# Performance work log

Measured on AMD Instinct MI355X. Metric: run time of the kernel, lower is better.

The kernel has to match this reference:

```python
import jax, jax.numpy as jnp
import numpy as np


def setup_inputs() -> dict:
    key = jax.random.key(0)
    ks = jax.random.split(key, 5)
    B, D, W = 8, 768, 128
    scale = 1.0 / np.sqrt(D)
    return {
        "x": jax.random.normal(ks[0], (B, D, W, W), dtype=jnp.float32),
        "in_proj_w": jax.random.normal(ks[1], (3 * D, D), dtype=jnp.float32) * scale,
        "in_proj_b": jax.random.normal(ks[2], (3 * D,), dtype=jnp.float32) * 0.01,
        "out_w": jax.random.normal(ks[3], (D, D), dtype=jnp.float32) * scale,
        "out_b": jax.random.normal(ks[4], (D,), dtype=jnp.float32) * 0.01,
        "num_heads": 12,
        "num_tokens": 8,
    }


def reference(x, in_proj_w, in_proj_b, out_w, out_b, num_heads, num_tokens):
    B, D, Wd, Hd = x.shape
    nt = num_tokens
    gs = Hd // nt            # grid (block) size
    T = nt * nt              # number of blocks / queries
    S = gs * gs              # k/v tokens per block
    h = num_heads
    hd = D // h

    # ---- query: adaptive avg pool to (nt, nt), flatten, permute -> (B, T, D)
    q = x.reshape(B, D, nt, gs, nt, gs).mean(axis=(3, 5))      # (B, D, nt, nt)
    q = q.reshape(B, D, T).transpose(0, 2, 1)                   # (B, T, D)

    # ---- key/value: faithful reproduction of unfold + view(x.size()) + reshape
    # torch: kv_perm (B,W,H,D) -> unfold -> (B, nt, nt, D, gs, gs) contiguous,
    # then reinterpreted flat as (B, W*H, D) (scrambles channel/pixel layout).
    t = x.transpose(0, 2, 3, 1)                                 # (B, W, H, D)
    t = t.reshape(B, nt, gs, nt, gs, D).transpose(0, 1, 3, 5, 2, 4)  # (B,nt,nt,D,gs,gs)
    kv = t.reshape(B, T, S, D)                                  # chunked into T blocks of S tokens

    # ---- in-projections (torch MultiheadAttention packed weights)
    Wq, Wk, Wv = in_proj_w[:D], in_proj_w[D:2 * D], in_proj_w[2 * D:]
    bq, bk, bv = in_proj_b[:D], in_proj_b[D:2 * D], in_proj_b[2 * D:]
    qp = (q @ Wq.T + bq).reshape(B, T, h, hd)                   # (B, T, h, hd)
    kp = (kv @ Wk.T + bk).reshape(B, T, S, h, hd)               # (B, T, S, h, hd)
    vp = (kv @ Wv.T + bv).reshape(B, T, S, h, hd)

    # ---- block-local single-query attention, batched over all T blocks
    scores = jnp.einsum("bthd,btshd->bths", qp, kp) / np.sqrt(hd)  # (B, T, h, S)
    attn = jax.nn.softmax(scores, axis=-1)
    ctx = jnp.einsum("bths,btshd->bthd", attn, vp).reshape(B, T, D)

    # ---- out projection
    return ctx @ out_w.T + out_b                                # (B, T, D)
```

## Files before the change

### kernel.cpp

```cpp
#include <hip/hip_runtime.h>
#include <hip/hip_bf16.h>

#define D_ 768
#define W_ 128
#define T_ 64
#define S_ 256
#define H_ 12
#define BT_ 512

typedef __attribute__((ext_vector_type(8))) short short8v;
typedef __attribute__((ext_vector_type(4))) float f32x4;

__device__ __forceinline__ unsigned short f2bf(float f) {
  unsigned u = __float_as_uint(f);
  u = (u + 0x7FFFu + ((u >> 16) & 1u)) >> 16;
  return (unsigned short)u;
}
__device__ __forceinline__ float bfu(unsigned s) {
  return __uint_as_float(s << 16);
}

__global__ __launch_bounds__(384) void k_pack(const float* __restrict__ x,
                                              unsigned short* __restrict__ packed,
                                              float* __restrict__ q) {
  const int blk  = blockIdx.x;
  const int cc   = blk & 15;
  const int tjp  = (blk >> 4) & 3;
  const int ti   = (blk >> 6) & 7;
  const int b    = blk >> 9;
  const int tid  = threadIdx.x;
  const int c8   = tid & 7;
  const int ch   = tid >> 3;
  const int btl  = c8 >> 2;
  const int btg0 = b*64 + ti*8 + tjp*2;
  const int ch0  = cc * 48;

  __shared__ unsigned short tile[48][2][264];
  __shared__ float poolsc[48][2];

  const float* xcol = x + (size_t)b*D_*16384 + (size_t)(ch0 + ch)*16384
                        + (16*ti)*128 + 32*tjp + c8*4;

  float psum = 0.f;
  #pragma unroll
  for (int r = 0; r < 16; ++r) {
    const float4 v = *(const float4*)(xcol + r*128);
    const int px = r*16 + (c8 & 3)*4;
    unsigned lo = (unsigned)f2bf(v.x) | ((unsigned)f2bf(v.y) << 16);
    unsigned hi = (unsigned)f2bf(v.z) | ((unsigned)f2bf(v.w) << 16);
    *(uint2*)&tile[ch][btl][px] = make_uint2(lo, hi);
    psum += (v.x + v.y) + (v.z + v.w);
  }
  psum += __shfl_xor(psum, 1);
  psum += __shfl_xor(psum, 2);
  if ((c8 & 3) == 0) poolsc[ch][btl] = psum;
  __syncthreads();

  for (int ii = tid; ii < 3072; ii += 384) {
    const int btl2 = ii / 1536;
    const int r2   = ii - btl2*1536;
    const int sl   = r2 / 96;
    const int r3   = r2 - sl*96;
    const int c    = r3 >> 5;
    const int p8   = r3 & 31;
    const int chs  = sl*3 + c;
    const uint4 v = *(const uint4*)&tile[chs][btl2][p8*8];
    unsigned short* dst = packed + (size_t)(btg0 + btl2)*(S_*D_)
                        + (size_t)(cc*16 + sl)*D_ + c*256 + p8*8;
    *(uint4*)dst = v;
  }
  if (tid < 96) {
    const int ch2 = tid >> 1, bl = tid & 1;
    q[(size_t)(btg0 + bl)*D_ + ch0 + ch2] = poolsc[ch2][bl] * (1.0f/256.0f);
  }
}

__global__ __launch_bounds__(256) void k_qp(const float* __restrict__ q,
                                            const float* __restrict__ ipw,
                                            const float* __restrict__ ipb,
                                            float* __restrict__ qp) {
  const int jt = blockIdx.x >> 6;
  const int bt0 = (blockIdx.x & 63) * 8;
  const int tid = threadIdx.x;
  const float* Wr = ipw + (size_t)jt*64*D_;
  __shared__ float wt[64][65];
  __shared__ float at[8][65];
  const int i = tid & 63, qw = tid >> 6;
  float acc[2] = {0,0};
  for (int dc = 0; dc < D_; dc += 64) {
    #pragma unroll
    for (int k = 0; k < 4; ++k) {
      const int idx = k*256 + tid;
      const int r = idx >> 4, c4 = idx & 15;
      *(float4*)&wt[r][c4*4] = *(const float4*)(Wr + (size_t)r*D_ + dc + c4*4);
    }
    if (tid < 128) {
      const int r = tid >> 4, c4 = tid & 15;
      *(float4*)&at[r][c4*4] = *(const float4*)(q + (size_t)(bt0 + r)*D_ + dc + c4*4);
    }
    __syncthreads();
    #pragma unroll
    for (int dd = 0; dd < 64; ++dd) {
      const float wv = wt[i][dd];
      #pragma unroll
      for (int k = 0; k < 2; ++k)
        acc[k] += at[qw + k*4][dd] * wv;
    }
    __syncthreads();
  }
  const float bqv = ipb[jt*64 + i];
  #pragma unroll
  for (int k = 0; k < 2; ++k)
    qp[(size_t)(bt0 + qw + k*4)*D_ + jt*64 + i] = acc[k] + bqv;
}

__global__ __launch_bounds__(256) void k_fold(const float* __restrict__ qp,
                                              const float* __restrict__ ipw,
                                              unsigned short* __restrict__ qkout) {
  const int btc = blockIdx.x & 15;
  const int nt  = blockIdx.x >> 4;
  const int h   = nt / 12;
  const int ddc = (nt % 12) * 64;
  const int bt0 = btc * 32;
  const int tid = threadIdx.x;
  __shared__ float qpl[32][68];
  __shared__ float wkl[64][68];
  #pragma unroll
  for (int k = 0; k < 2; ++k) {
    const int idx = k*256 + tid;
    const int r = idx >> 4, c4 = idx & 15;
    *(float4*)&qpl[r][c4*4] = *(const float4*)(qp + (size_t)(bt0 + r)*D_ + h*64 + c4*4);
  }
  #pragma unroll
  for (int k = 0; k < 4; ++k) {
    const int idx = k*256 + tid;
    const int r = idx >> 4, c4 = idx & 15;
    *(float4*)&wkl[r][c4*4] = *(const float4*)(ipw + (size_t)(D_ + h*64 + r)*D_ + ddc + c4*4);
  }
  __syncthreads();
  const int i = tid & 63, qw = tid >> 6;
  float acc[8] = {0,0,0,0,0,0,0,0};
  #pragma unroll 8
  for (int kk = 0; kk < 64; ++kk) {
    const float w = wkl[kk][i];
    #pragma unroll
    for (int k = 0; k < 8; ++k)
      acc[k] += qpl[qw + k*4][kk] * w;
  }
  #pragma unroll
  for (int k = 0; k < 8; ++k)
    qkout[((size_t)(bt0 + qw + k*4)*H_ + h)*D_ + ddc + i] = f2bf(acc[k] * 0.125f);
}

__global__ __launch_bounds__(512) void k_attn4(const unsigned short* __restrict__ packed,
                                               const unsigned short* __restrict__ qkin,
                                               unsigned short* __restrict__ wout) {
  const int bt = blockIdx.x;
  const int tid = threadIdx.x;
  const int wv = tid >> 6, lane = tid & 63;
  __shared__ float sc[12][260];

  const int m16 = lane & 15;
  const int kg  = lane >> 4;
  const unsigned short* pbase = packed + (size_t)bt * (S_*D_);

  {
    const int hB = (m16 < 12) ? m16 : 0;
    const unsigned short* qb  = qkin + ((size_t)bt*H_ + hB)*D_ + kg*8;
    const unsigned short* pA0 = pbase + (size_t)(wv*32      + m16)*D_ + kg*8;
    const unsigned short* pA1 = pbase + (size_t)(wv*32 + 16 + m16)*D_ + kg*8;
    f32x4 acc0 = {0.f,0.f,0.f,0.f};
    f32x4 acc1 = {0.f,0.f,0.f,0.f};
    #pragma unroll 4
    for (int ks = 0; ks < 24; ++ks) {
      const short8v b  = *(const short8v*)(qb  + ks*32);
      const short8v a0 = *(const short8v*)(pA0 + ks*32);
      const short8v a1 = *(const short8v*)(pA1 + ks*32);
      acc0 = __builtin_amdgcn_mfma_f32_16x16x32_bf16(a0, b, acc0, 0, 0, 0);
      acc1 = __builtin_amdgcn_mfma_f32_16x16x32_bf16(a1, b, acc1, 0, 0, 0);
    }
    if (m16 < 12) {
      #pragma unroll
      for (int r = 0; r < 4; ++r) {
        sc[m16][wv*32      + kg*4 + r] = acc0[r];
        sc[m16][wv*32 + 16 + kg*4 + r] = acc1[r];
      }
    }
  }
  __syncthreads();

  #pragma unroll
  for (int pass = 0; pass < 2; ++pass) {
    if (pass == 0 || wv < 4) {
      const int h = (pass == 0) ? wv : 8 + wv;
      float4 v = *(const float4*)(&sc[h][lane*4]);
      float m = fmaxf(fmaxf(v.x, v.y), fmaxf(v.z, v.w));
      #pragma unroll
      for (int off = 32; off > 0; off >>= 1) m = fmaxf(m, __shfl_xor(m, off));
      const float e0 = __expf(v.x - m), e1 = __expf(v.y - m),
                  e2 = __expf(v.z - m), e3 = __expf(v.w - m);
      float ss = (e0+e1)+(e2+e3);
      #pragma unroll
      for (int off = 32; off > 0; off >>= 1) ss += __shfl_xor(ss, off);
      const float inv = 1.0f / ss;
      *(float4*)(&sc[h][lane*4]) = make_float4(e0*inv, e1*inv, e2*inv, e3*inv);
    }
  }
  __syncthreads();

  if (tid < 384) {
    const int hb  = (tid / 96) * 3;
    const int dd8 = (tid - (hb/3)*96) * 8;
    float wacc[3][8];
    #pragma unroll
    for (int hh = 0; hh < 3; ++hh)
      #pragma unroll
      for (int j = 0; j < 8; ++j) wacc[hh][j] = 0.f;
    const unsigned short* pr = pbase + dd8;
    uint4 cur = *(const uint4*)pr;
    #pragma unroll 2
    for (int s = 0; s < 256; ++s) {
      uint4 nx = make_uint4(0,0,0,0);
      if (s < 255) nx = *(const uint4*)(pr + (size_t)(s + 1)*D_);
      float f[8];
      f[0] = bfu(cur.x & 0xFFFFu); f[1] = bfu(cur.x >> 16);
      f[2] = bfu(cur.y & 0xFFFFu); f[3] = bfu(cur.y >> 16);
      f[4] = bfu(cur.z & 0xFFFFu); f[5] = bfu(cur.z >> 16);
      f[6] = bfu(cur.w & 0xFFFFu); f[7] = bfu(cur.w >> 16);
      const float a0 = sc[hb + 0][s];
      const float a1 = sc[hb + 1][s];
      const float a2 = sc[hb + 2][s];
      #pragma unroll
      for (int j = 0; j < 8; ++j) {
        wacc[0][j] += a0 * f[j];
        wacc[1][j] += a1 * f[j];
        wacc[2][j] += a2 * f[j];
      }
      cur = nx;
    }
    unsigned short* wp = wout + ((size_t)bt*H_ + hb)*D_ + dd8;
    #pragma unroll
    for (int hh = 0; hh < 3; ++hh) {
      uint4 o;
      o.x = (unsigned)f2bf(wacc[hh][0]) | ((unsigned)f2bf(wacc[hh][1]) << 16);
      o.y = (unsigned)f2bf(wacc[hh][2]) | ((unsigned)f2bf(wacc[hh][3]) << 16);
      o.z = (unsigned)f2bf(wacc[hh][4]) | ((unsigned)f2bf(wacc[hh][5]) << 16);
      o.w = (unsigned)f2bf(wacc[hh][6]) | ((unsigned)f2bf(wacc[hh][7]) << 16);
      *(uint4*)(wp + (size_t)hh*D_) = o;
    }
  }
}

__global__ __launch_bounds__(256) void k_ctx(const unsigned short* __restrict__ wbuf,
                                             const float* __restrict__ ipw,
                                             const float* __restrict__ ipb,
                                             float* __restrict__ ctx) {
  const int h = blockIdx.x >> 6;
  const int bt0 = (blockIdx.x & 63) * 8;
  const int tid = threadIdx.x;
  const float* Wv = ipw + (size_t)2*D_*D_ + (size_t)h*64*D_;
  __shared__ float wt[64][65];
  __shared__ float at[8][65];
  const int i = tid & 63, qw = tid >> 6;
  float acc[2] = {0,0};
  for (int dc = 0; dc < D_; dc += 64) {
    #pragma unroll
    for (int k = 0; k < 4; ++k) {
      const int idx = k*256 + tid;
      const int r = idx >> 4, c4 = idx & 15;
      *(float4*)&wt[r][c4*4] = *(const float4*)(Wv + (size_t)r*D_ + dc + c4*4);
    }
    if (tid < 128) {
      const int r = tid >> 4, c4 = tid & 15;
      const uint2 v = *(const uint2*)(wbuf + ((size_t)(bt0 + r)*H_ + h)*D_ + dc + c4*4);
      at[r][c4*4 + 0] = bfu(v.x & 0xFFFFu);
      at[r][c4*4 + 1] = bfu(v.x >> 16);
      at[r][c4*4 + 2] = bfu(v.y & 0xFFFFu);
      at[r][c4*4 + 3] = bfu(v.y >> 16);
    }
    __syncthreads();
    #pragma unroll
    for (int dd = 0; dd < 64; ++dd) {
      const float wv = wt[i][dd];
      #pragma unroll
      for (int k = 0; k < 2; ++k)
        acc[k] += at[qw + k*4][dd] * wv;
    }
    __syncthreads();
  }
  const float bvv = ipb[2*D_ + h*64 + i];
  #pragma unroll
  for (int k = 0; k < 2; ++k)
    ctx[(size_t)(bt0 + qw + k*4)*D_ + h*64 + i] = acc[k] + bvv;
}

__global__ __launch_bounds__(256) void k_out(const float* __restrict__ ctx,
                                             const float* __restrict__ ow,
                                             const float* __restrict__ ob,
                                             float* __restrict__ out) {
  const int jt = blockIdx.x >> 6;
  const int bt0 = (blockIdx.x & 63) * 8;
  const int tid = threadIdx.x;
  const float* Wr = ow + (size_t)jt*64*D_;
  __shared__ float wt[64][65];
  __shared__ float at[8][65];
  const int i = tid & 63, qw = tid >> 6;
  float acc[2] = {0,0};
  for (int dc = 0; dc < D_; dc += 64) {
    #pragma unroll
    for (int k = 0; k < 4; ++k) {
      const int idx = k*256 + tid;
      const int r = idx >> 4, c4 = idx & 15;
      *(float4*)&wt[r][c4*4] = *(const float4*)(Wr + (size_t)r*D_ + dc + c4*4);
    }
    if (tid < 128) {
      const int r = tid >> 4, c4 = tid & 15;
      *(float4*)&at[r][c4*4] = *(const float4*)(ctx + (size_t)(bt0 + r)*D_ + dc + c4*4);
    }
    __syncthreads();
    #pragma unroll
    for (int dd = 0; dd < 64; ++dd) {
      const float wv = wt[i][dd];
      #pragma unroll
      for (int k = 0; k < 2; ++k)
        acc[k] += at[qw + k*4][dd] * wv;
    }
    __syncthreads();
  }
  const float obv = ob[jt*64 + i];
  #pragma unroll
  for (int k = 0; k < 2; ++k)
    out[(size_t)(bt0 + qw + k*4)*D_ + jt*64 + i] = acc[k] + obv;
}

__global__ __launch_bounds__(256) void k_q(const float* __restrict__ x, float* __restrict__ q) {
  const int bd = blockIdx.x;
  const int tid = threadIdx.x;
  const float4* xp = (const float4*)(x + (size_t)bd * (W_*W_));
  float acc[8] = {0,0,0,0,0,0,0,0};
  #pragma unroll
  for (int k = 0; k < 16; ++k) {
    float4 v = xp[k*256 + tid];
    acc[k>>1] += (v.x + v.y) + (v.z + v.w);
  }
  __shared__ float part[256][9];
  #pragma unroll
  for (int i = 0; i < 8; ++i) part[tid][i] = acc[i];
  __syncthreads();
  if (tid < 64) {
    const int ti = tid >> 3, tj = tid & 7;
    float s = 0.f;
    #pragma unroll
    for (int m = 0; m < 8; ++m)
      #pragma unroll
      for (int n = 0; n < 4; ++n)
        s += part[m*32 + tj*4 + n][ti];
    const int b = bd / D_, d = bd - b*D_;
    q[(size_t)(b*T_ + tid)*D_ + d] = s * (1.0f/256.0f);
  }
}

__global__ __launch_bounds__(256) void k_attn(const float* __restrict__ x,
                                              const unsigned short* __restrict__ qkin,
                                              unsigned short* __restrict__ wout) {
  const int bt = blockIdx.x;
  const int b = bt >> 6, t = bt & 63;
  const int ti = t >> 3, tj = t & 7;
  const int tid = threadIdx.x;
  __shared__ float qkl[H_*D_];
  __shared__ float sc[H_][S_];
  const float* xb = x + (size_t)b*D_*W_*W_ + ti*16*W_ + tj*16;
  {
    const uint4* src = (const uint4*)(qkin + (size_t)bt*H_*D_);
    #pragma unroll
    for (int k = 0; k < 5; ++k) {
      const int idx = k*256 + tid;
      if (idx < 1152) {
        const uint4 v = src[idx];
        float* d = qkl + idx*8;
        d[0] = bfu(v.x & 0xFFFFu); d[1] = bfu(v.x >> 16);
        d[2] = bfu(v.y & 0xFFFFu); d[3] = bfu(v.y >> 16);
        d[4] = bfu(v.z & 0xFFFFu); d[5] = bfu(v.z >> 16);
        d[6] = bfu(v.w & 0xFFFFu); d[7] = bfu(v.w >> 16);
      }
    }
  }
  __syncthreads();
  float acc[H_];
  #pragma unroll
  for (int h = 0; h < H_; ++h) acc[h] = 0.f;
  #pragma unroll
  for (int c = 0; c < 3; ++c) {
    const float* chp = xb + (size_t)(3*tid + c)*(W_*W_);
    for (int blk = 0; blk < 8; ++blk) {
      float4 v[8];
      #pragma unroll
      for (int u = 0; u < 8; ++u) {
        const int pg = blk*8 + u;
        v[u] = *(const float4*)(chp + (pg>>2)*W_ + (pg&3)*4);
      }
      const int dbase = c*256 + blk*32;
      #pragma unroll
      for (int h = 0; h < H_; ++h) {
        const float4* qh = (const float4*)(qkl + h*D_ + dbase);
        float s0 = 0.f;
        #pragma unroll
        for (int u = 0; u < 8; ++u) {
          const float4 qq = qh[u];
          s0 += qq.x*v[u].x + qq.y*v[u].y + qq.z*v[u].z + qq.w*v[u].w;
        }
        acc[h] += s0;
      }
    }
  }
  #pragma unroll
  for (int h = 0; h < H_; ++h) sc[h][tid] = acc[h];
  __syncthreads();
  {
    const int wv = tid >> 6, lane = tid & 63;
    #pragma unroll
    for (int hh = 0; hh < 3; ++hh) {
      const int h = wv*3 + hh;
      float4 v = *(const float4*)(&sc[h][lane*4]);
      float m = fmaxf(fmaxf(v.x, v.y), fmaxf(v.z, v.w));
      #pragma unroll
      for (int off = 32; off > 0; off >>= 1) m = fmaxf(m, __shfl_xor(m, off));
      const float e0 = __expf(v.x - m), e1 = __expf(v.y - m),
                  e2 = __expf(v.z - m), e3 = __expf(v.w - m);
      float ss = (e0+e1)+(e2+e3);
      #pragma unroll
      for (int off = 32; off > 0; off >>= 1) ss += __shfl_xor(ss, off);
      const float inv = 1.0f / ss;
      *(float4*)(&sc[h][lane*4]) = make_float4(e0*inv, e1*inv, e2*inv, e3*inv);
    }
  }
  __syncthreads();
  float wacc[H_][3];
  #pragma unroll
  for (int h = 0; h < H_; ++h) { wacc[h][0]=0.f; wacc[h][1]=0.f; wacc[h][2]=0.f; }
  const float* xp0 = xb + (tid>>4)*W_ + (tid&15);
  for (int s = 0; s < S_; ++s) {
    const float p0 = xp0[(size_t)(3*s+0)*(W_*W_)];
    const float p1 = xp0[(size_t)(3*s+1)*(W_*W_)];
    const float p2 = xp0[(size_t)(3*s+2)*(W_*W_)];
    #pragma unroll
    for (int h = 0; h < H_; ++h) {
      const float at = sc[h][s];
      wacc[h][0] += at*p0; wacc[h][1] += at*p1; wacc[h][2] += at*p2;
    }
  }
  unsigned short* wp = wout + (size_t)bt*H_*D_;
  #pragma unroll
  for (int h = 0; h < H_; ++h)
    #pragma unroll
    for (int c = 0; c < 3; ++c)
      wp[h*D_ + c*256 + tid] = f2bf(wacc[h][c]);
}

extern "C" void kernel_launch(void* const* d_in, const int* in_sizes, int n_in,
                              void* d_out, int out_size, void* d_ws, size_t ws_size,
                              hipStream_t stream) {
  const float* x   = (const float*)d_in[0];
  const float* ipw = (const float*)d_in[1];
  const float* ipb = (const float*)d_in[2];
  const float* ow  = (const float*)d_in[3];
  const float* ob  = (const float*)d_in[4];
  float* out = (float*)d_out;

  float* q    = (float*)d_ws;
  float* qp   = q    + (size_t)BT_*D_;
  unsigned short* qk = (unsigned short*)(qp + (size_t)BT_*D_);
  unsigned short* wb = (unsigned short*)(qp + (size_t)BT_*D_ + (size_t)BT_*H_*D_);
  float* ctxb = qp + (size_t)BT_*D_ + (size_t)BT_*H_*D_*2;
  unsigned short* packed = (unsigned short*)(ctxb + (size_t)BT_*D_);

  const size_t need_main = ((size_t)BT_*D_*3 + (size_t)BT_*H_*D_*2) * 4
                         + (size_t)BT_*D_*S_*2;

  if (ws_size >= need_main) {
    k_pack <<<dim3(4096), dim3(384), 0, stream>>>(x, packed, q);
    k_qp   <<<dim3(768),  dim3(256), 0, stream>>>(q, ipw, ipb, qp);
    k_fold <<<dim3(2304), dim3(256), 0, stream>>>(qp, ipw, qk);
    k_attn4<<<dim3(BT_),  dim3(512), 0, stream>>>(packed, qk, wb);
    k_ctx  <<<dim3(768),  dim3(256), 0, stream>>>(wb, ipw, ipb, ctxb);
    k_out  <<<dim3(768),  dim3(256), 0, stream>>>(ctxb, ow, ob, out);
  } else {
    k_q    <<<dim3(8*D_), dim3(256), 0, stream>>>(x, q);
    k_qp   <<<dim3(768),  dim3(256), 0, stream>>>(q, ipw, ipb, qp);
    k_fold <<<dim3(2304), dim3(256), 0, stream>>>(qp, ipw, qk);
    k_attn <<<dim3(BT_),  dim3(256), 0, stream>>>(x, qk, wb);
    k_ctx  <<<dim3(768),  dim3(256), 0, stream>>>(wb, ipw, ipb, ctxb);
    k_out  <<<dim3(768),  dim3(256), 0, stream>>>(ctxb, ow, ob, out);
  }
}
```

Before: 342.8 us.

## Stage KV tiles in LDS with online softmax in attention; halve GEMM column tiles

The attention kernel now streams the 256 packed key/value rows through LDS in 32-row tiles, prefetching the next tile into registers. It computes scores with MFMA from LDS and uses an online-softmax (running max and sum with rescale) so each tile is read from global memory once and reused for both the score and weighted-sum phases. The ctx and out projection kernels use 32-column weight tiles and twice as many blocks to raise parallelism. The cost is more barriers per tile, larger LDS use per block, and more redundant activation loads in the projections.

```diff
diff --git a/kernel.cpp b/kernel.cpp
--- a/kernel.cpp
+++ b/kernel.cpp
@@ -152,101 +152,141 @@
     qkout[((size_t)(bt0 + qw + k*4)*H_ + h)*D_ + ddc + i] = f2bf(acc[k] * 0.125f);
 }
 
-__global__ __launch_bounds__(512) void k_attn4(const unsigned short* __restrict__ packed,
+__global__ __launch_bounds__(512) void k_attn5(const unsigned short* __restrict__ packed,
                                                const unsigned short* __restrict__ qkin,
                                                unsigned short* __restrict__ wout) {
   const int bt = blockIdx.x;
   const int tid = threadIdx.x;
   const int wv = tid >> 6, lane = tid & 63;
-  __shared__ float sc[12][260];
-
-  const int m16 = lane & 15;
-  const int kg  = lane >> 4;
+  const int m16 = lane & 15, kg = lane >> 4;
+
+  __shared__ unsigned short tile[32][776];
+  __shared__ unsigned short qk_lds[12][776];
+  __shared__ float sc_part[4][12][32];
+  __shared__ float ptile[12][32];
+  __shared__ float mstate[12], lstate[12], alpha_s[12];
+
   const unsigned short* pbase = packed + (size_t)bt * (S_*D_);
 
   {
-    const int hB = (m16 < 12) ? m16 : 0;
-    const unsigned short* qb  = qkin + ((size_t)bt*H_ + hB)*D_ + kg*8;
-    const unsigned short* pA0 = pbase + (size_t)(wv*32      + m16)*D_ + kg*8;
-    const unsigned short* pA1 = pbase + (size_t)(wv*32 + 16 + m16)*D_ + kg*8;
-    f32x4 acc0 = {0.f,0.f,0.f,0.f};
-    f32x4 acc1 = {0.f,0.f,0.f,0.f};
-    #pragma unroll 4
-    for (int ks = 0; ks < 24; ++ks) {
-      const short8v b  = *(const short8v*)(qb  + ks*32);
-      const short8v a0 = *(const short8v*)(pA0 + ks*32);
-      const short8v a1 = *(const short8v*)(pA1 + ks*32);
-      acc0 = __builtin_amdgcn_mfma_f32_16x16x32_bf16(a0, b, acc0, 0, 0, 0);
-      acc1 = __builtin_amdgcn_mfma_f32_16x16x32_bf16(a1, b, acc1, 0, 0, 0);
-    }
-    if (m16 < 12) {
-      #pragma unroll
-      for (int r = 0; r < 4; ++r) {
-        sc[m16][wv*32      + kg*4 + r] = acc0[r];
-        sc[m16][wv*32 + 16 + kg*4 + r] = acc1[r];
-      }
-    }
-  }
-  __syncthreads();
-
-  #pragma unroll
-  for (int pass = 0; pass < 2; ++pass) {
-    if (pass == 0 || wv < 4) {
-      const int h = (pass == 0) ? wv : 8 + wv;
-      float4 v = *(const float4*)(&sc[h][lane*4]);
-      float m = fmaxf(fmaxf(v.x, v.y), fmaxf(v.z, v.w));
-      #pragma unroll
-      for (int off = 32; off > 0; off >>= 1) m = fmaxf(m, __shfl_xor(m, off));
-      const float e0 = __expf(v.x - m), e1 = __expf(v.y - m),
-                  e2 = __expf(v.z - m), e3 = __expf(v.w - m);
-      float ss = (e0+e1)+(e2+e3);
-      #pragma unroll
-      for (int off = 32; off > 0; off >>= 1) ss += __shfl_xor(ss, off);
-      const float inv = 1.0f / ss;
-      *(float4*)(&sc[h][lane*4]) = make_float4(e0*inv, e1*inv, e2*inv, e3*inv);
-    }
-  }
-  __syncthreads();
-
-  if (tid < 384) {
-    const int hb  = (tid / 96) * 3;
-    const int dd8 = (tid - (hb/3)*96) * 8;
-    float wacc[3][8];
-    #pragma unroll
-    for (int hh = 0; hh < 3; ++hh)
-      #pragma unroll
-      for (int j = 0; j < 8; ++j) wacc[hh][j] = 0.f;
-    const unsigned short* pr = pbase + dd8;
-    uint4 cur = *(const uint4*)pr;
-    #pragma unroll 2
-    for (int s = 0; s < 256; ++s) {
-      uint4 nx = make_uint4(0,0,0,0);
-      if (s < 255) nx = *(const uint4*)(pr + (size_t)(s + 1)*D_);
-      float f[8];
-      f[0] = bfu(cur.x & 0xFFFFu); f[1] = bfu(cur.x >> 16);
-      f[2] = bfu(cur.y & 0xFFFFu); f[3] = bfu(cur.y >> 16);
-      f[4] = bfu(cur.z & 0xFFFFu); f[5] = bfu(cur.z >> 16);
-      f[6] = bfu(cur.w & 0xFFFFu); f[7] = bfu(cur.w >> 16);
-      const float a0 = sc[hb + 0][s];
-      const float a1 = sc[hb + 1][s];
-      const float a2 = sc[hb + 2][s];
-      #pragma unroll
-      for (int j = 0; j < 8; ++j) {
-        wacc[0][j] += a0 * f[j];
-        wacc[1][j] += a1 * f[j];
-        wacc[2][j] += a2 * f[j];
-      }
-      cur = nx;
-    }
-    unsigned short* wp = wout + ((size_t)bt*H_ + hb)*D_ + dd8;
+    const unsigned short* qsrc = qkin + (size_t)bt*H_*D_;
+    for (int idx = tid; idx < 1152; idx += 512) {
+      const int e = idx*8;
+      const int row = e/768, col = e - row*768;
+      *(uint4*)&qk_lds[row][col] = *(const uint4*)(qsrc + e);
+    }
+    if (tid < 12) { mstate[tid] = -1e30f; lstate[tid] = 0.f; }
+  }
+
+  const int pr_r   = tid >> 4;
+  const int pr_off = (tid & 15) * 48;
+  uint4 pre[6];
+  {
+    const unsigned short* src = pbase + (size_t)pr_r*768 + pr_off;
+    #pragma unroll
+    for (int k = 0; k < 6; ++k) pre[k] = *(const uint4*)(src + k*8);
+  }
+
+  float wacc[3][6];
+  #pragma unroll
+  for (int a = 0; a < 3; ++a)
+    #pragma unroll
+    for (int b = 0; b < 6; ++b) wacc[a][b] = 0.f;
+
+  const int hb  = tid >> 7;
+  const int dd  = (tid & 127) * 6;
+  const int m2  = wv & 1, kq = wv >> 1;
+  const int hB  = (m16 < 12) ? m16 : 11;
+
+  for (int t = 0; t < 8; ++t) {
+    __syncthreads();
+    #pragma unroll
+    for (int k = 0; k < 6; ++k)
+      *(uint4*)&tile[pr_r][pr_off + k*8] = pre[k];
+    __syncthreads();
+
+    if (t < 7) {
+      const unsigned short* src = pbase + (size_t)(t+1)*32*768 + (size_t)pr_r*768 + pr_off;
+      #pragma unroll
+      for (int k = 0; k < 6; ++k) pre[k] = *(const uint4*)(src + k*8);
+    }
+
+    {
+      f32x4 acc = {0.f, 0.f, 0.f, 0.f};
+      #pragma unroll
+      for (int ks = 0; ks < 6; ++ks) {
+        const int d = kq*192 + ks*32 + kg*8;
+        const short8v a = *(const short8v*)&tile[m2*16 + m16][d];
+        const short8v b = *(const short8v*)&qk_lds[hB][d];
+        acc = __builtin_amdgcn_mfma_f32_16x16x32_bf16(a, b, acc, 0, 0, 0);
+      }
+      if (m16 < 12) {
+        #pragma unroll
+        for (int r = 0; r < 4; ++r)
+          sc_part[kq][m16][m2*16 + kg*4 + r] = acc[r];
+      }
+    }
+    __syncthreads();
+
+    if (tid < 384) {
+      const int h = tid >> 5, si = tid & 31;
+      const float s4 = sc_part[0][h][si] + sc_part[1][h][si]
+                     + sc_part[2][h][si] + sc_part[3][h][si];
+      float tm = s4;
+      #pragma unroll
+      for (int off = 16; off > 0; off >>= 1) tm = fmaxf(tm, __shfl_xor(tm, off));
+      const float mo = mstate[h];
+      const float nm = fmaxf(mo, tm);
+      const float p = __expf(s4 - nm);
+      float ps = p;
+      #pragma unroll
+      for (int off = 16; off > 0; off >>= 1) ps += __shfl_xor(ps, off);
+      ptile[h][si] = p;
+      if (si == 0) {
+        const float al = __expf(mo - nm);
+        alpha_s[h] = al;
+        lstate[h] = lstate[h]*al + ps;
+        mstate[h] = nm;
+      }
+    }
+    __syncthreads();
+
+    {
+      const float a0 = alpha_s[hb*3+0], a1 = alpha_s[hb*3+1], a2 = alpha_s[hb*3+2];
+      #pragma unroll
+      for (int j = 0; j < 6; ++j) { wacc[0][j]*=a0; wacc[1][j]*=a1; wacc[2][j]*=a2; }
+      #pragma unroll 4
+      for (int si = 0; si < 32; ++si) {
+        const unsigned short* tp = &tile[si][dd];
+        const unsigned u0 = *(const unsigned*)(tp);
+        const unsigned u1 = *(const unsigned*)(tp + 2);
+        const unsigned u2 = *(const unsigned*)(tp + 4);
+        float f[6];
+        f[0] = bfu(u0 & 0xFFFFu); f[1] = bfu(u0 >> 16);
+        f[2] = bfu(u1 & 0xFFFFu); f[3] = bfu(u1 >> 16);
+        f[4] = bfu(u2 & 0xFFFFu); f[5] = bfu(u2 >> 16);
+        const float p0 = ptile[hb*3+0][si];
+        const float p1 = ptile[hb*3+1][si];
+        const float p2 = ptile[hb*3+2][si];
+        #pragma unroll
+        for (int j = 0; j < 6; ++j) {
+          wacc[0][j] += p0*f[j]; wacc[1][j] += p1*f[j]; wacc[2][j] += p2*f[j];
+        }
+      }
+    }
+  }
+
+  {
     #pragma unroll
     for (int hh = 0; hh < 3; ++hh) {
-      uint4 o;
-      o.x = (unsigned)f2bf(wacc[hh][0]) | ((unsigned)f2bf(wacc[hh][1]) << 16);
-      o.y = (unsigned)f2bf(wacc[hh][2]) | ((unsigned)f2bf(wacc[hh][3]) << 16);
-      o.z = (unsigned)f2bf(wacc[hh][4]) | ((unsigned)f2bf(wacc[hh][5]) << 16);
-      o.w = (unsigned)f2bf(wacc[hh][6]) | ((unsigned)f2bf(wacc[hh][7]) << 16);
-      *(uint4*)(wp + (size_t)hh*D_) = o;
+      const float linv = 1.0f / lstate[hb*3 + hh];
+      unsigned short* wp = wout + ((size_t)bt*H_ + hb*3 + hh)*D_ + dd;
+      unsigned v0 = (unsigned)f2bf(wacc[hh][0]*linv) | ((unsigned)f2bf(wacc[hh][1]*linv) << 16);
+      unsigned v1 = (unsigned)f2bf(wacc[hh][2]*linv) | ((unsigned)f2bf(wacc[hh][3]*linv) << 16);
+      unsigned v2 = (unsigned)f2bf(wacc[hh][4]*linv) | ((unsigned)f2bf(wacc[hh][5]*linv) << 16);
+      *(unsigned*)(wp)     = v0;
+      *(unsigned*)(wp + 2) = v1;
+      *(unsigned*)(wp + 4) = v2;
     }
   }
 }
@@ -255,17 +295,19 @@
                                              const float* __restrict__ ipw,
                                              const float* __restrict__ ipb,
                                              float* __restrict__ ctx) {
-  const int h = blockIdx.x >> 6;
-  const int bt0 = (blockIdx.x & 63) * 8;
-  const int tid = threadIdx.x;
-  const float* Wv = ipw + (size_t)2*D_*D_ + (size_t)h*64*D_;
-  __shared__ float wt[64][65];
+  const int h   = blockIdx.x >> 7;
+  const int rem = blockIdx.x & 127;
+  const int ih  = rem >> 6;
+  const int bt0 = (rem & 63) * 8;
+  const int tid = threadIdx.x;
+  const float* Wv = ipw + (size_t)(2*D_ + h*64 + ih*32)*D_;
+  __shared__ float wt[32][65];
   __shared__ float at[8][65];
-  const int i = tid & 63, qw = tid >> 6;
-  float acc[2] = {0,0};
+  const int j = tid & 31, grp = tid >> 5;
+  float acc = 0.f;
   for (int dc = 0; dc < D_; dc += 64) {
     #pragma unroll
-    for (int k = 0; k < 4; ++k) {
+    for (int k = 0; k < 2; ++k) {
       const int idx = k*256 + tid;
       const int r = idx >> 4, c4 = idx & 15;
       *(float4*)&wt[r][c4*4] = *(const float4*)(Wv + (size_t)r*D_ + dc + c4*4);
@@ -280,35 +322,29 @@
     }
     __syncthreads();
     #pragma unroll
-    for (int dd = 0; dd < 64; ++dd) {
-      const float wv = wt[i][dd];
-      #pragma unroll
-      for (int k = 0; k < 2; ++k)
-        acc[k] += at[qw + k*4][dd] * wv;
-    }
-    __syncthreads();
-  }
-  const float bvv = ipb[2*D_ + h*64 + i];
-  #pragma unroll
-  for (int k = 0; k < 2; ++k)
-    ctx[(size_t)(bt0 + qw + k*4)*D_ + h*64 + i] = acc[k] + bvv;
+    for (int dd = 0; dd < 64; ++dd)
+      acc += at[grp][dd] * wt[j][dd];
+    __syncthreads();
+  }
+  const int col = h*64 + ih*32 + j;
+  ctx[(size_t)(bt0 + grp)*D_ + col] = acc + ipb[2*D_ + col];
 }
 
 __global__ __launch_bounds__(256) void k_out(const float* __restrict__ ctx,
                                              const float* __restrict__ ow,
                                              const float* __restrict__ ob,
                                              float* __restrict__ out) {
-  const int jt = blockIdx.x >> 6;
+  const int ct  = blockIdx.x >> 6;
   const int bt0 = (blockIdx.x & 63) * 8;
   const int tid = threadIdx.x;
-  const float* Wr = ow + (size_t)jt*64*D_;
-  __shared__ float wt[64][65];
+  const float* Wr = ow + (size_t)ct*32*D_;
+  __shared__ float wt[32][65];
   __shared__ float at[8][65];
-  const int i = tid & 63, qw = tid >> 6;
-  float acc[2] = {0,0};
+  const int j = tid & 31, grp = tid >> 5;
+  float acc = 0.f;
   for (int dc = 0; dc < D_; dc += 64) {
     #pragma unroll
-    for (int k = 0; k < 4; ++k) {
+    for (int k = 0; k < 2; ++k) {
       const int idx = k*256 + tid;
       const int r = idx >> 4, c4 = idx & 15;
       *(float4*)&wt[r][c4*4] = *(const float4*)(Wr + (size_t)r*D_ + dc + c4*4);
@@ -319,18 +355,12 @@
     }
     __syncthreads();
     #pragma unroll
-    for (int dd = 0; dd < 64; ++dd) {
-      const float wv = wt[i][dd];
-      #pragma unroll
-      for (int k = 0; k < 2; ++k)
-        acc[k] += at[qw + k*4][dd] * wv;
-    }
-    __syncthreads();
-  }
-  const float obv = ob[jt*64 + i];
-  #pragma unroll
-  for (int k = 0; k < 2; ++k)
-    out[(size_t)(bt0 + qw + k*4)*D_ + jt*64 + i] = acc[k] + obv;
+    for (int dd = 0; dd < 64; ++dd)
+      acc += at[grp][dd] * wt[j][dd];
+    __syncthreads();
+  }
+  const int col = ct*32 + j;
+  out[(size_t)(bt0 + grp)*D_ + col] = acc + ob[col];
 }
 
 __global__ __launch_bounds__(256) void k_q(const float* __restrict__ x, float* __restrict__ q) {
@@ -481,15 +511,15 @@
     k_pack <<<dim3(4096), dim3(384), 0, stream>>>(x, packed, q);
     k_qp   <<<dim3(768),  dim3(256), 0, stream>>>(q, ipw, ipb, qp);
     k_fold <<<dim3(2304), dim3(256), 0, stream>>>(qp, ipw, qk);
-    k_attn4<<<dim3(BT_),  dim3(512), 0, stream>>>(packed, qk, wb);
-    k_ctx  <<<dim3(768),  dim3(256), 0, stream>>>(wb, ipw, ipb, ctxb);
-    k_out  <<<dim3(768),  dim3(256), 0, stream>>>(ctxb, ow, ob, out);
+    k_attn5<<<dim3(BT_),  dim3(512), 0, stream>>>(packed, qk, wb);
+    k_ctx  <<<dim3(1536), dim3(256), 0, stream>>>(wb, ipw, ipb, ctxb);
+    k_out  <<<dim3(1536), dim3(256), 0, stream>>>(ctxb, ow, ob, out);
   } else {
     k_q    <<<dim3(8*D_), dim3(256), 0, stream>>>(x, q);
     k_qp   <<<dim3(768),  dim3(256), 0, stream>>>(q, ipw, ipb, qp);
     k_fold <<<dim3(2304), dim3(256), 0, stream>>>(qp, ipw, qk);
     k_attn <<<dim3(BT_),  dim3(256), 0, stream>>>(x, qk, wb);
-    k_ctx  <<<dim3(768),  dim3(256), 0, stream>>>(wb, ipw, ipb, ctxb);
-    k_out  <<<dim3(768),  dim3(256), 0, stream>>>(ctxb, ow, ob, out);
-  }
-}
+    k_ctx  <<<dim3(1536), dim3(256), 0, stream>>>(wb, ipw, ipb, ctxb);
+    k_out  <<<dim3(1536), dim3(256), 0, stream>>>(ctxb, ow, ob, out);
+  }
+}
```

After: 366.6 us. 1.07x slower.
